# Performance work log

Hardware: AMD Instinct MI355X
Metric: run time of the kernel (lower is better)

The kernel has to match this reference:

```python
import jax, jax.numpy as jnp
import numpy as np
import math

D_MODEL = 1024
NUM_HEADS = 16
HEAD_DIM = D_MODEL // NUM_HEADS


def setup_inputs() -> dict:
    key = jax.random.key(0)
    ks = jax.random.split(key, 9)
    B, S = 2, 2048
    scale = 1.0 / math.sqrt(D_MODEL)
    x = jax.random.normal(ks[0], (B, S, D_MODEL), dtype=jnp.float32)
    # torch nn.Linear params: weight [out, in], bias [out]
    Wq = jax.random.normal(ks[1], (D_MODEL, D_MODEL), dtype=jnp.float32) * scale
    bq = jax.random.normal(ks[2], (D_MODEL,), dtype=jnp.float32) * scale
    Wk = jax.random.normal(ks[3], (D_MODEL, D_MODEL), dtype=jnp.float32) * scale
    bk = jax.random.normal(ks[4], (D_MODEL,), dtype=jnp.float32) * scale
    Wv = jax.random.normal(ks[5], (D_MODEL, D_MODEL), dtype=jnp.float32) * scale
    bv = jax.random.normal(ks[6], (D_MODEL,), dtype=jnp.float32) * scale
    Wo = jax.random.normal(ks[7], (D_MODEL, D_MODEL), dtype=jnp.float32) * scale
    bo = jax.random.normal(ks[8], (D_MODEL,), dtype=jnp.float32) * scale
    return {"x": x, "Wq": Wq, "bq": bq, "Wk": Wk, "bk": bk,
            "Wv": Wv, "bv": bv, "Wo": Wo, "bo": bo}


def reference(x, Wq, bq, Wk, bk, Wv, bv, Wo, bo):
    B, S, _ = x.shape
    H, Dh = NUM_HEADS, HEAD_DIM

    def proj(W, b):
        # torch Linear: x @ W.T + b -> [B,S,D] -> [B,H,S,Dh]
        y = jnp.einsum('bsd,ed->bse', x, W) + b
        return y.reshape(B, S, H, Dh).transpose(0, 2, 1, 3)

    Q = proj(Wq, bq)
    K = proj(Wk, bk)
    V = proj(Wv, bv)

    # scores [B,H,S,S], causal mask with -inf, then scale by 1/sqrt(head_dim)
    scores = jnp.einsum('bhqd,bhkd->bhqk', Q, K)
    causal = jnp.tril(jnp.ones((S, S), dtype=bool))
    scores = jnp.where(causal, scores, -jnp.inf)
    A = jax.nn.softmax(scores / math.sqrt(Dh), axis=-1)

    O = jnp.einsum('bhqk,bhkd->bhqd', A, V)  # [B,H,S,Dh]
    O = O.transpose(0, 2, 1, 3).reshape(B, S, H * Dh)
    return jnp.einsum('bsd,ed->bse', O, Wo) + bo
```

## Files before the change

kernel.cpp:

```cpp
#include <hip/hip_runtime.h>


typedef _Float16 f16x8 __attribute__((ext_vector_type(8)));
typedef _Float16 f16x4 __attribute__((ext_vector_type(4)));
typedef _Float16 f16x2 __attribute__((ext_vector_type(2)));
typedef float f32x4 __attribute__((ext_vector_type(4)));

#define S_  2048
#define DM  1024
#define NH  16
#define DH  64

__device__ __forceinline__ void gload_lds16(const void* g, void* s) {
  __builtin_amdgcn_global_load_lds(
      (const __attribute__((address_space(1))) void*)g,
      (__attribute__((address_space(3))) void*)s, 16, 0, 0);
}

__device__ __forceinline__ f16x2 pkrtz(float a, float b) {
  return __builtin_bit_cast(f16x2, __builtin_amdgcn_cvt_pkrtz(a, b));
}


__global__ void cvt_all_kernel(const float* __restrict__ x,
                               const float* __restrict__ w0,
                               const float* __restrict__ w1,
                               const float* __restrict__ w2,
                               const float* __restrict__ w3,
                               _Float16* __restrict__ xb,
                               _Float16* __restrict__ wb) {
  const int bid = blockIdx.x;
  const float* src;
  _Float16* dst;
  int idx;
  if (bid < 4096) {
    src = x; dst = xb; idx = bid * 256 + threadIdx.x;
  } else {
    const int j = bid - 4096;
    const int y = j >> 10;
    src = (y == 0) ? w0 : (y == 1) ? w1 : (y == 2) ? w2 : w3;
    dst = wb + (size_t)y * (DM * DM);
    idx = (j & 1023) * 256 + threadIdx.x;
  }
  const float4 v = ((const float4*)src)[idx];
  f16x4 h;
  h[0] = (_Float16)v.x; h[1] = (_Float16)v.y;
  h[2] = (_Float16)v.z; h[3] = (_Float16)v.w;
  ((f16x4*)dst)[idx] = h;
}


__global__ __launch_bounds__(256, 2) void gemm_qkv_kernel(
    const _Float16* __restrict__ xb, const _Float16* __restrict__ wb,
    const float* __restrict__ bq, const float* __restrict__ bk,
    const float* __restrict__ bv, _Float16* __restrict__ qkv)
{
  __shared__ _Float16 As[2][128 * 32];
  __shared__ _Float16 Ws[2][128 * 32];
  const int z = blockIdx.z;
  const _Float16* W = wb + (size_t)z * (DM * DM);
  const float* bias = (z == 0) ? bq : ((z == 1) ? bk : bv);
  _Float16* out = qkv + (size_t)z * 4194304;

  const f32x4 z4 = {0.f, 0.f, 0.f, 0.f};
  f32x4 acc[4][4];
#pragma unroll
  for (int mi = 0; mi < 4; ++mi)
#pragma unroll
    for (int ni = 0; ni < 4; ++ni) acc[mi][ni] = z4;

  const int m0 = blockIdx.y * 128, n0 = blockIdx.x * 128;
  const int t = threadIdx.x;
  const int w = t >> 6, l = t & 63;
  const int quad = l >> 4, ln = l & 15;
  const int wm = (w >> 1) << 6, wn = (w & 1) << 6;
  const int srow = l >> 2, scol = (l & 3) << 3;

  for (int k0 = 0; k0 < DM; k0 += 64) {
#pragma unroll
    for (int h = 0; h < 2; ++h)
#pragma unroll
      for (int i = 0; i < 2; ++i) {
        const int ra = w * 32 + i * 16;
        gload_lds16(&xb[(size_t)(m0 + ra + srow) * DM + k0 + h * 32 + scol],
                    &As[h][ra * 32]);
        gload_lds16(&W[(size_t)(n0 + ra + srow) * DM + k0 + h * 32 + scol],
                    &Ws[h][ra * 32]);
      }
    __syncthreads();

#pragma unroll
    for (int h = 0; h < 2; ++h) {
      f16x8 af[4], bf[4];
#pragma unroll
      for (int mi = 0; mi < 4; ++mi)
        af[mi] = *(const f16x8*)&As[h][(wm + mi * 16 + ln) * 32 + quad * 8];
#pragma unroll
      for (int ni = 0; ni < 4; ++ni)
        bf[ni] = *(const f16x8*)&Ws[h][(wn + ni * 16 + ln) * 32 + quad * 8];
#pragma unroll
      for (int mi = 0; mi < 4; ++mi)
#pragma unroll
        for (int ni = 0; ni < 4; ++ni)
          acc[mi][ni] = __builtin_amdgcn_mfma_f32_16x16x32_f16(
              af[mi], bf[ni], acc[mi][ni], 0, 0, 0);
    }
    __syncthreads();
  }

  const float scale = (z == 0) ? 0.18033688f : 1.0f;

#pragma unroll
  for (int ni = 0; ni < 4; ++ni) {
    const int c = n0 + wn + ni * 16 + ln;
    const float bias_c = bias[c];
    const int h = c >> 6, d = c & 63;
#pragma unroll
    for (int mi = 0; mi < 4; ++mi) {
      const int mb = m0 + wm + mi * 16 + quad * 4;
#pragma unroll
      for (int r = 0; r < 4; ++r) {
        const int mg = mb + r;
        const int b = mg >> 11, s = mg & 2047;
        const int bh = b * NH + h;
        const float v = (acc[mi][ni][r] + bias_c) * scale;
        size_t idx;
        if (z == 2)
          idx = (size_t)bh * 131072 + (s >> 5) * 2048 + (d >> 4) * 512 +
                ((s >> 3) & 3) * 128 + (d & 15) * 8 + (s & 7);
        else
          idx = (size_t)bh * 131072 + (s >> 4) * 1024 + (d >> 5) * 512 +
                ((d >> 3) & 3) * 128 + (s & 15) * 8 + (d & 7);
        out[idx] = (_Float16)v;
      }
    }
  }
}


__global__ __launch_bounds__(256, 2) void gemm_out_kernel(
    const _Float16* __restrict__ ob, const _Float16* __restrict__ wo,
    const float* __restrict__ bo, float* __restrict__ out)
{
  __shared__ _Float16 As[2][128 * 32];
  __shared__ _Float16 Ws[2][64 * 32];
  const f32x4 z4 = {0.f, 0.f, 0.f, 0.f};
  f32x4 acc[2][4];
#pragma unroll
  for (int mi = 0; mi < 2; ++mi)
#pragma unroll
    for (int ni = 0; ni < 4; ++ni) acc[mi][ni] = z4;

  const int m0 = blockIdx.y * 128, n0 = blockIdx.x * 64;
  const int t = threadIdx.x;
  const int w = t >> 6, l = t & 63;
  const int quad = l >> 4, ln = l & 15;
  const int srow = l >> 2, scol = (l & 3) << 3;

  for (int k0 = 0; k0 < DM; k0 += 64) {
#pragma unroll
    for (int h = 0; h < 2; ++h) {
#pragma unroll
      for (int i = 0; i < 2; ++i) {
        const int ra = w * 32 + i * 16;
        gload_lds16(&ob[(size_t)(m0 + ra + srow) * DM + k0 + h * 32 + scol],
                    &As[h][ra * 32]);
      }
      gload_lds16(&wo[(size_t)(n0 + w * 16 + srow) * DM + k0 + h * 32 + scol],
                  &Ws[h][w * 16 * 32]);
    }
    __syncthreads();

#pragma unroll
    for (int h = 0; h < 2; ++h) {
      f16x8 af[2], bf[4];
#pragma unroll
      for (int mi = 0; mi < 2; ++mi)
        af[mi] = *(const f16x8*)&As[h][(w * 32 + mi * 16 + ln) * 32 + quad * 8];
#pragma unroll
      for (int ni = 0; ni < 4; ++ni)
        bf[ni] = *(const f16x8*)&Ws[h][(ni * 16 + ln) * 32 + quad * 8];
#pragma unroll
      for (int mi = 0; mi < 2; ++mi)
#pragma unroll
        for (int ni = 0; ni < 4; ++ni)
          acc[mi][ni] = __builtin_amdgcn_mfma_f32_16x16x32_f16(
              af[mi], bf[ni], acc[mi][ni], 0, 0, 0);
    }
    __syncthreads();
  }

#pragma unroll
  for (int ni = 0; ni < 4; ++ni) {
    const int c = n0 + ni * 16 + ln;
    const float bias_c = bo[c];
#pragma unroll
    for (int mi = 0; mi < 2; ++mi) {
      const int mb = m0 + w * 32 + mi * 16 + quad * 4;
#pragma unroll
      for (int r = 0; r < 4; ++r)
        out[(size_t)(mb + r) * DM + c] = acc[mi][ni][r] + bias_c;
    }
  }
}


template <bool DIAG>
__device__ __forceinline__ void tile16(
    const _Float16* __restrict__ vb_, int t,
    const f16x8 (&kc)[4], const f16x8 (&qf)[2],
    f32x4 (&oacc)[4], float& l_i,
    _Float16* Ps, int quad, int ln, int l, int h)
{
  f16x8 vf[4];
#pragma unroll
  for (int i = 0; i < 4; ++i)
    vf[i] = *(const f16x8*)(vb_ + (size_t)(t * 4 + i) * 512 + l * 8);

  const f32x4 z4 = {0.f, 0.f, 0.f, 0.f};
  f32x4 sacc[2];
  sacc[0] = z4; sacc[1] = z4;

#pragma unroll
  for (int ks = 0; ks < 2; ++ks)
#pragma unroll
    for (int mi = 0; mi < 2; ++mi)
      sacc[mi] = __builtin_amdgcn_mfma_f32_16x16x32_f16(
          kc[mi * 2 + ks], qf[ks], sacc[mi], 0, 0, 0);

  const int sw = (ln & 3) << 1;
  float rs = 0.f;
#pragma unroll
  for (int mi = 0; mi < 2; ++mi) {
    float p[4];
#pragma unroll
    for (int r = 0; r < 4; ++r) {
      p[r] = __builtin_amdgcn_exp2f(sacc[mi][r]);
      if (DIAG && (mi * 16 + quad * 4 + r > h * 16 + ln)) p[r] = 0.f;
      rs += p[r];
    }
    const f16x2 lo = pkrtz(p[0], p[1]);
    const f16x2 hi = pkrtz(p[2], p[3]);
    const f16x4 pk = __builtin_shufflevector(lo, hi, 0, 1, 2, 3);
    const int g = (mi * 4 + quad) ^ sw;
    *(f16x4*)&Ps[ln * 40 + g * 4] = pk;
  }
  l_i += rs;

  const int g2 = (quad * 2) ^ sw;
  const f16x8 pb = *(const f16x8*)&Ps[ln * 40 + g2 * 4];

#pragma unroll
  for (int di = 0; di < 4; ++di)
    oacc[di] = __builtin_amdgcn_mfma_f32_16x16x32_f16(
        vf[di], pb, oacc[di], 0, 0, 0);
}

__global__ __launch_bounds__(256, 4) void attn_kernel(
    const _Float16* __restrict__ QF, const _Float16* __restrict__ KF,
    const _Float16* __restrict__ VF, _Float16* __restrict__ Ob)
{
  __shared__ _Float16 Ps[4 * 16 * 40];

  const int i = blockIdx.x;
  const int bh = ((i & 7) << 2) | ((i >> 3) & 3);
  const int p = i >> 5;

  const int tid = threadIdx.x;
  const int w = tid >> 6, l = tid & 63;
  const int quad = l >> 4, ln = l & 15;

  const int role = (w + (i >> 8)) & 3;
  const int qw = (role < 2) ? (63 - p) : p;
  const int h = role & 1;

  const _Float16* qb_ = QF + (size_t)bh * 131072;
  const _Float16* kb_ = KF + (size_t)bh * 131072;
  const _Float16* vb_ = VF + (size_t)bh * 131072;
  _Float16* psw = Ps + w * (16 * 40);
  const int bidx = bh >> 4, hh = bh & 15;

  f16x8 qf[2];
#pragma unroll
  for (int ks = 0; ks < 2; ++ks)
    qf[ks] = *(const f16x8*)
        (qb_ + (size_t)((qw * 2 + h) * 2 + ks) * 512 + l * 8);

  const f32x4 z4 = {0.f, 0.f, 0.f, 0.f};
  f32x4 oacc[4];
#pragma unroll
  for (int di = 0; di < 4; ++di) oacc[di] = z4;
  float l_i = 0.f;

  f16x8 kc[4];
#pragma unroll
  for (int ii = 0; ii < 4; ++ii)
    kc[ii] = *(const f16x8*)(kb_ + (size_t)ii * 512 + l * 8);

  for (int t = 0; t < qw; ++t) {
    f16x8 kn[4];
#pragma unroll
    for (int ii = 0; ii < 4; ++ii)
      kn[ii] = *(const f16x8*)
          (kb_ + (size_t)((t + 1) * 4 + ii) * 512 + l * 8);
    tile16<false>(vb_, t, kc, qf, oacc, l_i, psw, quad, ln, l, h);
#pragma unroll
    for (int ii = 0; ii < 4; ++ii) kc[ii] = kn[ii];
  }
  tile16<true>(vb_, qw, kc, qf, oacc, l_i, psw, quad, ln, l, h);

  l_i += __shfl_xor(l_i, 16);
  l_i += __shfl_xor(l_i, 32);
  const float inv = 1.0f / l_i;

  const int q = qw * 32 + h * 16 + ln;
  _Float16* orow = Ob + (size_t)(bidx * S_ + q) * DM + hh * DH + quad * 4;
#pragma unroll
  for (int di = 0; di < 4; ++di) {
    f16x4 o4;
#pragma unroll
    for (int r = 0; r < 4; ++r)
      o4[r] = (_Float16)(oacc[di][r] * inv);
    *(f16x4*)(orow + di * 16) = o4;
  }
}


extern "C" void kernel_launch(void* const* d_in, const int* in_sizes, int n_in,
                              void* d_out, int out_size, void* d_ws, size_t ws_size,
                              hipStream_t stream) {
  (void)in_sizes; (void)n_in; (void)out_size; (void)ws_size;
  const float* x  = (const float*)d_in[0];
  const float* Wq = (const float*)d_in[1];
  const float* bq = (const float*)d_in[2];
  const float* Wk = (const float*)d_in[3];
  const float* bk = (const float*)d_in[4];
  const float* Wv = (const float*)d_in[5];
  const float* bv = (const float*)d_in[6];
  const float* Wo = (const float*)d_in[7];
  const float* bo = (const float*)d_in[8];

  char* ws = (char*)d_ws;
  _Float16* xb  = (_Float16*)(ws);
  _Float16* wb  = (_Float16*)(ws + (8u << 20));
  _Float16* qkv = (_Float16*)(ws + (16u << 20));
  _Float16* ob  = (_Float16*)(ws + (40u << 20));

  cvt_all_kernel<<<dim3(8192), dim3(256), 0, stream>>>(x, Wq, Wk, Wv, Wo, xb, wb);
  gemm_qkv_kernel<<<dim3(8, 32, 3), dim3(256), 0, stream>>>(xb, wb, bq, bk, bv, qkv);
  attn_kernel<<<dim3(1024), dim3(256), 0, stream>>>(
      qkv, qkv + 4194304, qkv + 2 * 4194304, ob);
  gemm_out_kernel<<<dim3(16, 32), dim3(256), 0, stream>>>(
      ob, wb + (size_t)3 * DM * DM, bo, (float*)d_out);
}
```

Measured before the change: 187.0 us.

## Split KV range across wave pairs with LDS merge in attention kernel

Each query tile is now processed by two waves that take even and odd KV tiles, and their partial outputs and row sums are merged through shared memory. Each block handles the complementary tiles 63-p and p in two phases. This is meant to shorten the serial per-wave KV loop and balance causal work. The P-tile LDS layout also changes from an XOR swizzle with a 40-element stride to a rotated slot layout with a 64-element stride. The cost is extra LDS, a block-wide sync per phase, and more LDS footprint that may limit occupancy.

Measured after the change: 183.2 us. 1.02x faster.

```diff
diff --git a/kernel.cpp b/kernel.cpp
--- a/kernel.cpp
+++ b/kernel.cpp
@@ -228,7 +228,6 @@
       sacc[mi] = __builtin_amdgcn_mfma_f32_16x16x32_f16(
           kc[mi * 2 + ks], qf[ks], sacc[mi], 0, 0, 0);
 
-  const int sw = (ln & 3) << 1;
   float rs = 0.f;
 #pragma unroll
   for (int mi = 0; mi < 2; ++mi) {
@@ -242,13 +241,13 @@
     const f16x2 lo = pkrtz(p[0], p[1]);
     const f16x2 hi = pkrtz(p[2], p[3]);
     const f16x4 pk = __builtin_shufflevector(lo, hi, 0, 1, 2, 3);
-    const int g = (mi * 4 + quad) ^ sw;
-    *(f16x4*)&Ps[ln * 40 + g * 4] = pk;
+    const int slot = ((mi * 4 + quad) + 2 * ln) & 15;
+    *(f16x4*)&Ps[ln * 64 + slot * 4] = pk;
   }
   l_i += rs;
 
-  const int g2 = (quad * 2) ^ sw;
-  const f16x8 pb = *(const f16x8*)&Ps[ln * 40 + g2 * 4];
+  const int slot2 = ((quad * 2) + 2 * ln) & 15;
+  const f16x8 pb = *(const f16x8*)&Ps[ln * 64 + slot2 * 4];
 
 #pragma unroll
   for (int di = 0; di < 4; ++di)
@@ -256,11 +255,85 @@
         vf[di], pb, oacc[di], 0, 0, 0);
 }
 
+__device__ __forceinline__ void run_phase(
+    const _Float16* __restrict__ qb_, const _Float16* __restrict__ kb_,
+    const _Float16* __restrict__ vb_, _Float16* __restrict__ Ob,
+    _Float16* psw, float* mO, float* mL,
+    int qtile, int h, int e, int quad, int ln, int l,
+    int bidx, int hh)
+{
+  f16x8 qf[2];
+#pragma unroll
+  for (int ks = 0; ks < 2; ++ks)
+    qf[ks] = *(const f16x8*)
+        (qb_ + (size_t)((qtile * 2 + h) * 2 + ks) * 512 + l * 8);
+
+  const f32x4 z4 = {0.f, 0.f, 0.f, 0.f};
+  f32x4 oacc[4];
+#pragma unroll
+  for (int di = 0; di < 4; ++di) oacc[di] = z4;
+  float l_i = 0.f;
+
+  const int a = qtile;
+  int t = e;
+  if (t <= a) {
+    f16x8 kc[4];
+#pragma unroll
+    for (int ii = 0; ii < 4; ++ii)
+      kc[ii] = *(const f16x8*)(kb_ + (size_t)(t * 4 + ii) * 512 + l * 8);
+    while (t + 2 <= a) {
+      f16x8 kn[4];
+#pragma unroll
+      for (int ii = 0; ii < 4; ++ii)
+        kn[ii] = *(const f16x8*)
+            (kb_ + (size_t)((t + 2) * 4 + ii) * 512 + l * 8);
+      tile16<false>(vb_, t, kc, qf, oacc, l_i, psw, quad, ln, l, h);
+#pragma unroll
+      for (int ii = 0; ii < 4; ++ii) kc[ii] = kn[ii];
+      t += 2;
+    }
+    if (t == a)
+      tile16<true>(vb_, t, kc, qf, oacc, l_i, psw, quad, ln, l, h);
+    else
+      tile16<false>(vb_, t, kc, qf, oacc, l_i, psw, quad, ln, l, h);
+  }
+
+  if (e) {
+#pragma unroll
+    for (int di = 0; di < 4; ++di)
+      *(f32x4*)&mO[di * 256 + l * 4] = oacc[di];
+    mL[l] = l_i;
+  }
+  __syncthreads();
+  if (!e) {
+#pragma unroll
+    for (int di = 0; di < 4; ++di)
+      oacc[di] += *(const f32x4*)&mO[di * 256 + l * 4];
+    l_i += mL[l];
+    l_i += __shfl_xor(l_i, 16);
+    l_i += __shfl_xor(l_i, 32);
+    const float inv = 1.0f / l_i;
+
+    const int q = qtile * 32 + h * 16 + ln;
+    _Float16* orow = Ob + (size_t)(bidx * S_ + q) * DM + hh * DH + quad * 4;
+#pragma unroll
+    for (int di = 0; di < 4; ++di) {
+      f16x4 o4;
+#pragma unroll
+      for (int r = 0; r < 4; ++r)
+        o4[r] = (_Float16)(oacc[di][r] * inv);
+      *(f16x4*)(orow + di * 16) = o4;
+    }
+  }
+}
+
 __global__ __launch_bounds__(256, 4) void attn_kernel(
     const _Float16* __restrict__ QF, const _Float16* __restrict__ KF,
     const _Float16* __restrict__ VF, _Float16* __restrict__ Ob)
 {
-  __shared__ _Float16 Ps[4 * 16 * 40];
+  __shared__ _Float16 Ps[4 * 16 * 64];
+  __shared__ float mrgO[2][2][1024];
+  __shared__ float mrgL[2][2][64];
 
   const int i = blockIdx.x;
   const int bh = ((i & 7) << 2) | ((i >> 3) & 3);
@@ -269,60 +342,19 @@
   const int tid = threadIdx.x;
   const int w = tid >> 6, l = tid & 63;
   const int quad = l >> 4, ln = l & 15;
-
-  const int role = (w + (i >> 8)) & 3;
-  const int qw = (role < 2) ? (63 - p) : p;
-  const int h = role & 1;
+  const int h = w >> 1;
+  const int e = w & 1;
 
   const _Float16* qb_ = QF + (size_t)bh * 131072;
   const _Float16* kb_ = KF + (size_t)bh * 131072;
   const _Float16* vb_ = VF + (size_t)bh * 131072;
-  _Float16* psw = Ps + w * (16 * 40);
+  _Float16* psw = Ps + w * (16 * 64);
   const int bidx = bh >> 4, hh = bh & 15;
 
-  f16x8 qf[2];
-#pragma unroll
-  for (int ks = 0; ks < 2; ++ks)
-    qf[ks] = *(const f16x8*)
-        (qb_ + (size_t)((qw * 2 + h) * 2 + ks) * 512 + l * 8);
-
-  const f32x4 z4 = {0.f, 0.f, 0.f, 0.f};
-  f32x4 oacc[4];
-#pragma unroll
-  for (int di = 0; di < 4; ++di) oacc[di] = z4;
-  float l_i = 0.f;
-
-  f16x8 kc[4];
-#pragma unroll
-  for (int ii = 0; ii < 4; ++ii)
-    kc[ii] = *(const f16x8*)(kb_ + (size_t)ii * 512 + l * 8);
-
-  for (int t = 0; t < qw; ++t) {
-    f16x8 kn[4];
-#pragma unroll
-    for (int ii = 0; ii < 4; ++ii)
-      kn[ii] = *(const f16x8*)
-          (kb_ + (size_t)((t + 1) * 4 + ii) * 512 + l * 8);
-    tile16<false>(vb_, t, kc, qf, oacc, l_i, psw, quad, ln, l, h);
-#pragma unroll
-    for (int ii = 0; ii < 4; ++ii) kc[ii] = kn[ii];
-  }
-  tile16<true>(vb_, qw, kc, qf, oacc, l_i, psw, quad, ln, l, h);
-
-  l_i += __shfl_xor(l_i, 16);
-  l_i += __shfl_xor(l_i, 32);
-  const float inv = 1.0f / l_i;
-
-  const int q = qw * 32 + h * 16 + ln;
-  _Float16* orow = Ob + (size_t)(bidx * S_ + q) * DM + hh * DH + quad * 4;
-#pragma unroll
-  for (int di = 0; di < 4; ++di) {
-    f16x4 o4;
-#pragma unroll
-    for (int r = 0; r < 4; ++r)
-      o4[r] = (_Float16)(oacc[di][r] * inv);
-    *(f16x4*)(orow + di * 16) = o4;
-  }
+  run_phase(qb_, kb_, vb_, Ob, psw, &mrgO[0][h][0], &mrgL[0][h][0],
+            63 - p, h, e, quad, ln, l, bidx, hh);
+  run_phase(qb_, kb_, vb_, Ob, psw, &mrgO[1][h][0], &mrgL[1][h][0],
+            p, h, e, quad, ln, l, bidx, hh);
 }
 
 
```

## Split attention key range across wave pairs and merge partials through LDS

Applied to the files above, without the earlier changes.

The attention kernel now launches one block per 32-query tile. Pairs of waves split the key tiles between them by even and odd index, then the partial outputs and row sums are combined through shared memory before the final write. The grid doubles, and the load-balancing role mapping that paired long and short query tiles is removed. K and V loads move inside the tile routine without software prefetch, the P staging buffer uses a rotated 64-stride layout, and launch bounds rise to 6 blocks. It adds a block-wide sync and LDS merge traffic, and removing the K prefetch may expose load latency.

New measurement: 183.0 us. -2.1%, faster.

```diff
diff --git a/kernel.cpp b/kernel.cpp
--- a/kernel.cpp
+++ b/kernel.cpp
@@ -207,28 +207,30 @@
 
 template <bool DIAG>
 __device__ __forceinline__ void tile16(
-    const _Float16* __restrict__ vb_, int t,
-    const f16x8 (&kc)[4], const f16x8 (&qf)[2],
-    f32x4 (&oacc)[4], float& l_i,
+    const _Float16* __restrict__ kb_, const _Float16* __restrict__ vb_,
+    int t, const f16x8 (&qf)[2], f32x4 (&oacc)[4], float& l_i,
     _Float16* Ps, int quad, int ln, int l, int h)
 {
-  f16x8 vf[4];
-#pragma unroll
-  for (int i = 0; i < 4; ++i)
-    vf[i] = *(const f16x8*)(vb_ + (size_t)(t * 4 + i) * 512 + l * 8);
-
   const f32x4 z4 = {0.f, 0.f, 0.f, 0.f};
+  f16x8 kv[4];
+
+#pragma unroll
+  for (int ii = 0; ii < 4; ++ii)
+    kv[ii] = *(const f16x8*)(kb_ + (size_t)(t * 4 + ii) * 512 + l * 8);
+
   f32x4 sacc[2];
   sacc[0] = z4; sacc[1] = z4;
-
 #pragma unroll
   for (int ks = 0; ks < 2; ++ks)
 #pragma unroll
     for (int mi = 0; mi < 2; ++mi)
       sacc[mi] = __builtin_amdgcn_mfma_f32_16x16x32_f16(
-          kc[mi * 2 + ks], qf[ks], sacc[mi], 0, 0, 0);
-
-  const int sw = (ln & 3) << 1;
+          kv[mi * 2 + ks], qf[ks], sacc[mi], 0, 0, 0);
+
+#pragma unroll
+  for (int ii = 0; ii < 4; ++ii)
+    kv[ii] = *(const f16x8*)(vb_ + (size_t)(t * 4 + ii) * 512 + l * 8);
+
   float rs = 0.f;
 #pragma unroll
   for (int mi = 0; mi < 2; ++mi) {
@@ -242,49 +244,49 @@
     const f16x2 lo = pkrtz(p[0], p[1]);
     const f16x2 hi = pkrtz(p[2], p[3]);
     const f16x4 pk = __builtin_shufflevector(lo, hi, 0, 1, 2, 3);
-    const int g = (mi * 4 + quad) ^ sw;
-    *(f16x4*)&Ps[ln * 40 + g * 4] = pk;
+    const int slot = ((mi * 4 + quad) + 2 * ln) & 15;
+    *(f16x4*)&Ps[ln * 64 + slot * 4] = pk;
   }
   l_i += rs;
 
-  const int g2 = (quad * 2) ^ sw;
-  const f16x8 pb = *(const f16x8*)&Ps[ln * 40 + g2 * 4];
+  const int slot2 = ((quad * 2) + 2 * ln) & 15;
+  const f16x8 pb = *(const f16x8*)&Ps[ln * 64 + slot2 * 4];
 
 #pragma unroll
   for (int di = 0; di < 4; ++di)
     oacc[di] = __builtin_amdgcn_mfma_f32_16x16x32_f16(
-        vf[di], pb, oacc[di], 0, 0, 0);
-}
-
-__global__ __launch_bounds__(256, 4) void attn_kernel(
+        kv[di], pb, oacc[di], 0, 0, 0);
+}
+
+__global__ __launch_bounds__(256, 6) void attn_kernel(
     const _Float16* __restrict__ QF, const _Float16* __restrict__ KF,
     const _Float16* __restrict__ VF, _Float16* __restrict__ Ob)
 {
-  __shared__ _Float16 Ps[4 * 16 * 40];
+  __shared__ _Float16 Ps[4 * 16 * 64];
+  __shared__ float mrgO[2][1024];
+  __shared__ float mrgL[2][64];
 
   const int i = blockIdx.x;
-  const int bh = ((i & 7) << 2) | ((i >> 3) & 3);
-  const int p = i >> 5;
+  const int bh = i & 31;
+  const int a = 63 - (i >> 5);
 
   const int tid = threadIdx.x;
   const int w = tid >> 6, l = tid & 63;
   const int quad = l >> 4, ln = l & 15;
-
-  const int role = (w + (i >> 8)) & 3;
-  const int qw = (role < 2) ? (63 - p) : p;
-  const int h = role & 1;
+  const int h = w >> 1;
+  const int e = w & 1;
 
   const _Float16* qb_ = QF + (size_t)bh * 131072;
   const _Float16* kb_ = KF + (size_t)bh * 131072;
   const _Float16* vb_ = VF + (size_t)bh * 131072;
-  _Float16* psw = Ps + w * (16 * 40);
+  _Float16* psw = Ps + w * (16 * 64);
   const int bidx = bh >> 4, hh = bh & 15;
 
   f16x8 qf[2];
 #pragma unroll
   for (int ks = 0; ks < 2; ++ks)
     qf[ks] = *(const f16x8*)
-        (qb_ + (size_t)((qw * 2 + h) * 2 + ks) * 512 + l * 8);
+        (qb_ + (size_t)((a * 2 + h) * 2 + ks) * 512 + l * 8);
 
   const f32x4 z4 = {0.f, 0.f, 0.f, 0.f};
   f32x4 oacc[4];
@@ -292,36 +294,38 @@
   for (int di = 0; di < 4; ++di) oacc[di] = z4;
   float l_i = 0.f;
 
-  f16x8 kc[4];
-#pragma unroll
-  for (int ii = 0; ii < 4; ++ii)
-    kc[ii] = *(const f16x8*)(kb_ + (size_t)ii * 512 + l * 8);
-
-  for (int t = 0; t < qw; ++t) {
-    f16x8 kn[4];
-#pragma unroll
-    for (int ii = 0; ii < 4; ++ii)
-      kn[ii] = *(const f16x8*)
-          (kb_ + (size_t)((t + 1) * 4 + ii) * 512 + l * 8);
-    tile16<false>(vb_, t, kc, qf, oacc, l_i, psw, quad, ln, l, h);
-#pragma unroll
-    for (int ii = 0; ii < 4; ++ii) kc[ii] = kn[ii];
-  }
-  tile16<true>(vb_, qw, kc, qf, oacc, l_i, psw, quad, ln, l, h);
-
-  l_i += __shfl_xor(l_i, 16);
-  l_i += __shfl_xor(l_i, 32);
-  const float inv = 1.0f / l_i;
-
-  const int q = qw * 32 + h * 16 + ln;
-  _Float16* orow = Ob + (size_t)(bidx * S_ + q) * DM + hh * DH + quad * 4;
-#pragma unroll
-  for (int di = 0; di < 4; ++di) {
-    f16x4 o4;
-#pragma unroll
-    for (int r = 0; r < 4; ++r)
-      o4[r] = (_Float16)(oacc[di][r] * inv);
-    *(f16x4*)(orow + di * 16) = o4;
+  int t = e;
+  for (; t < a; t += 2)
+    tile16<false>(kb_, vb_, t, qf, oacc, l_i, psw, quad, ln, l, h);
+  if (t == a)
+    tile16<true>(kb_, vb_, t, qf, oacc, l_i, psw, quad, ln, l, h);
+
+  if (e) {
+#pragma unroll
+    for (int di = 0; di < 4; ++di)
+      *(f32x4*)&mrgO[h][di * 256 + l * 4] = oacc[di];
+    mrgL[h][l] = l_i;
+  }
+  __syncthreads();
+  if (!e) {
+#pragma unroll
+    for (int di = 0; di < 4; ++di)
+      oacc[di] += *(const f32x4*)&mrgO[h][di * 256 + l * 4];
+    l_i += mrgL[h][l];
+    l_i += __shfl_xor(l_i, 16);
+    l_i += __shfl_xor(l_i, 32);
+    const float inv = 1.0f / l_i;
+
+    const int q = a * 32 + h * 16 + ln;
+    _Float16* orow = Ob + (size_t)(bidx * S_ + q) * DM + hh * DH + quad * 4;
+#pragma unroll
+    for (int di = 0; di < 4; ++di) {
+      f16x4 o4;
+#pragma unroll
+      for (int r = 0; r < 4; ++r)
+        o4[r] = (_Float16)(oacc[di][r] * inv);
+      *(f16x4*)(orow + di * 16) = o4;
+    }
   }
 }
 
@@ -348,7 +352,7 @@
 
   cvt_all_kernel<<<dim3(8192), dim3(256), 0, stream>>>(x, Wq, Wk, Wv, Wo, xb, wb);
   gemm_qkv_kernel<<<dim3(8, 32, 3), dim3(256), 0, stream>>>(xb, wb, bq, bk, bv, qkv);
-  attn_kernel<<<dim3(1024), dim3(256), 0, stream>>>(
+  attn_kernel<<<dim3(2048), dim3(256), 0, stream>>>(
       qkv, qkv + 4194304, qkv + 2 * 4194304, ob);
   gemm_out_kernel<<<dim3(16, 32), dim3(256), 0, stream>>>(
       ob, wb + (size_t)3 * DM * DM, bo, (float*)d_out);
```
